# Kernel optimization log

Measured on AMD Instinct MI355X. Metric: run time of the kernel, lower is better.

The kernel has to match this reference:

```python
import jax, jax.numpy as jnp
import numpy as np

B, DIM, H, W = 8, 128, 64, 64
K = 7                      # involution kernel size
PAD = (K - 1) // 2
GC = 16                    # group_channels (RedNet involution default)
G = DIM // GC              # groups = 8
RED = 4                    # reduction_ratio
BN_EPS = 1e-5
LN_EPS = 1e-6


def setup_inputs() -> dict:
    key = jax.random.key(0)
    ks = jax.random.split(key, 8)
    s = lambda k, sh: jax.random.normal(k, sh, jnp.float32) * 0.02
    return {
        "x": jax.random.normal(ks[0], (B, DIM, H, W), jnp.float32),
        # involution kernel-generation branch: 1x1 conv -> BN -> ReLU -> 1x1 conv
        "conv1_w": s(ks[1], (DIM // RED, DIM)), "conv1_b": jnp.zeros((DIM // RED,), jnp.float32),
        "bn_g": jnp.ones((DIM // RED,), jnp.float32), "bn_b": jnp.zeros((DIM // RED,), jnp.float32),
        "bn_mean": jnp.zeros((DIM // RED,), jnp.float32), "bn_var": jnp.ones((DIM // RED,), jnp.float32),
        "conv2_w": s(ks[2], (K * K * G, DIM // RED)), "conv2_b": jnp.zeros((K * K * G,), jnp.float32),
        # LayerNorm (channels_last)
        "ln_g": jnp.ones((DIM,), jnp.float32), "ln_b": jnp.zeros((DIM,), jnp.float32),
        # pointwise MLP
        "pw1_w": s(ks[3], (2 * DIM, DIM)), "pw1_b": jnp.zeros((2 * DIM,), jnp.float32),
        "pw2_w": s(ks[4], (DIM, 2 * DIM)), "pw2_b": jnp.zeros((DIM,), jnp.float32),
    }


def _involution(x, conv1_w, conv1_b, bn_g, bn_b, bn_mean, bn_var, conv2_w, conv2_b):
    # kernel-generation: 1x1 conv -> BN(eval) -> ReLU -> 1x1 conv
    t = jnp.einsum('oc,bchw->bohw', conv1_w, x) + conv1_b[None, :, None, None]
    scale = bn_g * jax.lax.rsqrt(bn_var + BN_EPS)
    t = t * scale[None, :, None, None] + (bn_b - bn_mean * scale)[None, :, None, None]
    t = jax.nn.relu(t)
    wgt = jnp.einsum('oc,bchw->bohw', conv2_w, t) + conv2_b[None, :, None, None]
    wgt = wgt.reshape(B, G, K * K, H, W)            # per-pixel kernels
    # apply per-pixel kernel: accumulate over window offsets (no unfold materialization)
    xp = jnp.pad(x, ((0, 0), (0, 0), (PAD, PAD), (PAD, PAD)))
    xg = xp.reshape(B, G, GC, H + 2 * PAD, W + 2 * PAD)
    out = jnp.zeros((B, G, GC, H, W), x.dtype)
    for i in range(K):
        for j in range(K):
            patch = xg[:, :, :, i:i + H, j:j + W]   # [B,G,GC,H,W]
            out = out + wgt[:, :, i * K + j][:, :, None] * patch
    return out.reshape(B, DIM, H, W)


def reference(x, conv1_w, conv1_b, bn_g, bn_b, bn_mean, bn_var, conv2_w, conv2_b,
              ln_g, ln_b, pw1_w, pw1_b, pw2_w, pw2_b):
    identity = x
    y = _involution(x, conv1_w, conv1_b, bn_g, bn_b, bn_mean, bn_var, conv2_w, conv2_b)
    y = y.transpose(0, 2, 3, 1)                     # NCHW -> NHWC
    mu = jnp.mean(y, axis=-1, keepdims=True)
    var = jnp.var(y, axis=-1, keepdims=True)
    y = (y - mu) * jax.lax.rsqrt(var + LN_EPS) * ln_g + ln_b
    y = jnp.einsum('bhwc,fc->bhwf', y, pw1_w) + pw1_b
    y = jax.nn.gelu(y, approximate=False)           # torch nn.GELU default (erf)
    # dropout: inference mode -> identity
    y = jnp.einsum('bhwf,cf->bhwc', y, pw2_w) + pw2_b
    y = y.transpose(0, 3, 1, 2)                     # NHWC -> NCHW
    return y + identity
```

## Files before the change

### kernel.cpp

```cpp
#include <hip/hip_runtime.h>
#include <hip/hip_bf16.h>
#include <math.h>

#define Bn   8
#define DIM  128
#define Hs   64
#define Ws   64
#define PADn 3
#define GC   16
#define Gn   8
#define CMID 32
#define NW   392
#define NWP  416

typedef __bf16 bf16x8 __attribute__((ext_vector_type(8)));
typedef float  f32x4  __attribute__((ext_vector_type(4)));
typedef _Float16 h2v  __attribute__((ext_vector_type(2)));
typedef __fp16   fp16x2 __attribute__((ext_vector_type(2)));

__device__ __forceinline__ f32x4 mfma16(bf16x8 a, bf16x8 b, f32x4 c) {
    return __builtin_amdgcn_mfma_f32_16x16x32_bf16(a, b, c, 0, 0, 0);
}

__device__ __forceinline__ __bf16 tobf(float v) {
    __hip_bfloat16 h = __float2bfloat16(v);
    return *reinterpret_cast<__bf16*>(&h);
}

__device__ __forceinline__ unsigned su16(float f) {
    __hip_bfloat16 h = __float2bfloat16(f);
    return (unsigned)*reinterpret_cast<unsigned short*>(&h);
}

__device__ __forceinline__ unsigned pk2u(float a, float b) {
    fp16x2 p = __builtin_amdgcn_cvt_pkrtz(a, b);
    return __builtin_bit_cast(unsigned, p);
}

__device__ __forceinline__ float gelu_t(float v) {
    float u = 0.7978845608f * v * fmaf(0.044715f, v * v, 1.0f);
    float t = __builtin_amdgcn_exp2f(fminf(u, 30.f) * 2.885390082f);
    return v * t * __builtin_amdgcn_rcpf(t + 1.0f);
}

__global__ __launch_bounds__(256) void k0_cvt(const float* __restrict__ w1,
        const float* __restrict__ w2,
        const float* __restrict__ pw1, const float* __restrict__ pw2,
        const float* __restrict__ x,
        __hip_bfloat16* __restrict__ w1b, __hip_bfloat16* __restrict__ w2b,
        __hip_bfloat16* __restrict__ mw1b, __hip_bfloat16* __restrict__ mw2b,
        unsigned* __restrict__ xpair) {
    int T = blockIdx.x * 256 + threadIdx.x;
    if (T < 32768) {
        int i = T;
        if (i < CMID * DIM) w1b[i] = __float2bfloat16(w1[i]);
        if (i < NWP * CMID)
            w2b[i] = (i < NW * CMID) ? __float2bfloat16(w2[i]) : __float2bfloat16(0.f);
        {
            int f = i >> 7, j = i & 127;
            int qq = j >> 5, gg = (j >> 2) & 7, mm = j & 3;
            mw1b[i] = __float2bfloat16(pw1[f * 128 + gg * 16 + qq + 4 * mm]);
        }
        mw2b[i] = __float2bfloat16(pw2[i]);
    }
    int c8 = T >> 10;
    int p4 = (T & 1023) * 4;
    int bb = c8 >> 6, gg = (c8 >> 3) & 7, cc = c8 & 7;
    size_t src = ((size_t)(bb * DIM + gg * GC + cc)) * 4096 + p4;
    float4 lo = *(const float4*)&x[src];
    float4 hi = *(const float4*)&x[src + 8 * 4096];
    uint4 o;
    o.x = pk2u(lo.x, hi.x);
    o.y = pk2u(lo.y, hi.y);
    o.z = pk2u(lo.z, hi.z);
    o.w = pk2u(lo.w, hi.w);
    *(uint4*)&xpair[(size_t)c8 * 4096 + p4] = o;
}

__global__ __launch_bounds__(256) void k_all(const float* __restrict__ x,
        const unsigned* __restrict__ xpair,
        const __hip_bfloat16* __restrict__ w1b, const float* __restrict__ b1v,
        const float* __restrict__ bng, const float* __restrict__ bnb,
        const float* __restrict__ bnm, const float* __restrict__ bnv,
        const __hip_bfloat16* __restrict__ w2b, const float* __restrict__ b2v,
        const float* __restrict__ lng, const float* __restrict__ lnb,
        const __hip_bfloat16* __restrict__ mw1b, const float* __restrict__ mb1,
        const __hip_bfloat16* __restrict__ mw2b, const float* __restrict__ mb2,
        float* __restrict__ out) {
    __shared__ __align__(16) char uni[33792];
    __shared__ float ps[4][64], pss[4][64], mu_s[64], rs_s[64];
    h2v* xp    = (h2v*)uni;
    h2v* wgt2  = (h2v*)(uni + 16128);
    __hip_bfloat16* tsh = (__hip_bfloat16*)(uni + 29072);
    __hip_bfloat16* ylds = (__hip_bfloat16*)uni;
    __hip_bfloat16* zsh  = (__hip_bfloat16*)uni;

    int b = blockIdx.x & 7, h = blockIdx.x >> 3;
    int tid = threadIdx.x, lane = tid & 63, q = tid >> 6;
    int l15 = lane & 15, l4 = lane >> 4;
    int m0 = q * 16;

    int goff[16];
    unsigned ldsoPk[8];
#pragma unroll
    for (int e = 0; e < 16; ++e) {
        int i = tid + e * 256;
        int ccp = i / 490;
        int rem = i - ccp * 490;
        int r = rem / 70, col = rem - r * 70;
        int hh = h + r - PADn, wc = col - PADn;
        bool ok = (i < 3920) & ((unsigned)hh < (unsigned)Hs) & ((unsigned)wc < (unsigned)Ws);
        goff[e] = ok ? (ccp * 4096 + hh * 64 + wc) : -1;
        unsigned lo16 = (unsigned)(ccp * 504 + r * 72 + col);
        if ((e & 1) == 0) ldsoPk[e >> 1] = lo16;
        else              ldsoPk[e >> 1] |= lo16 << 16;
    }

    auto stage = [&](int g) {
        const unsigned* xg = xpair + (size_t)(b * 64 + g * 8) * 4096;
#pragma unroll
        for (int hf = 0; hf < 2; ++hf) {
            unsigned v[8];
#pragma unroll
            for (int e8 = 0; e8 < 8; ++e8) {
                int go = goff[hf * 8 + e8];
                v[e8] = (go >= 0) ? xg[go] : 0u;
            }
#pragma unroll
            for (int e8 = 0; e8 < 8; ++e8) {
                int e = hf * 8 + e8;
                if (e < 15 || tid < 80) {
                    unsigned ldso = (ldsoPk[e >> 1] >> ((e & 1) * 16)) & 0xFFFFu;
                    *(unsigned*)&xp[ldso] = v[e8];
                }
            }
        }
    };

    bf16x8 afr[4];
#pragma unroll
    for (int ks = 0; ks < 4; ++ks)
#pragma unroll
        for (int i = 0; i < 8; ++i) {
            int c = ks * 32 + l4 * 8 + i;
            afr[ks][i] = tobf(x[(((size_t)b * DIM + c) * Hs + h) * Ws + m0 + l15]);
        }
    f32x4 acc1[2];
    acc1[0] = (f32x4){0.f, 0.f, 0.f, 0.f};
    acc1[1] = (f32x4){0.f, 0.f, 0.f, 0.f};
#pragma unroll
    for (int nt = 0; nt < 2; ++nt)
#pragma unroll
        for (int ks = 0; ks < 4; ++ks) {
            bf16x8 bf = *(const bf16x8*)&w1b[(nt * 16 + l15) * DIM + ks * 32 + l4 * 8];
            acc1[nt] = mfma16(afr[ks], bf, acc1[nt]);
        }
#pragma unroll
    for (int nt = 0; nt < 2; ++nt) {
        int o = nt * 16 + l15;
        float sc = bng[o] * rsqrtf(bnv[o] + 1e-5f);
        float sh = bnb[o] - bnm[o] * sc;
        float bv = b1v[o];
#pragma unroll
        for (int r = 0; r < 4; ++r) {
            float v = (acc1[nt][r] + bv) * sc + sh;
            tsh[(m0 + l4 * 4 + r) * 34 + o] = __float2bfloat16(fmaxf(v, 0.f));
        }
    }
    __syncthreads();

    bf16x8 a_t = *(const bf16x8*)&tsh[(m0 + l15) * 34 + l4 * 8];

    unsigned ypk[16];
    float s = 0.f, ss = 0.f;

#pragma unroll 1
    for (int g = 0; g < Gn; ++g) {
        stage(g);
        {
            f32x4 ac[4];
#pragma unroll
            for (int nt = 0; nt < 4; ++nt) ac[nt] = (f32x4){0.f, 0.f, 0.f, 0.f};
#pragma unroll
            for (int nt = 0; nt < 4; ++nt) {
                bf16x8 bf = *(const bf16x8*)&w2b[(size_t)(g * 49 + nt * 16 + l15) * CMID + l4 * 8];
                ac[nt] = mfma16(a_t, bf, ac[nt]);
            }
#pragma unroll
            for (int nt = 0; nt < 4; ++nt) {
                int p = nt * 16 + l15;
                if (p < 49) {
                    float bias = b2v[g * 49 + p];
#pragma unroll
                    for (int r = 0; r < 4; ++r) {
                        _Float16 hf16 = (_Float16)(ac[nt][r] + bias);
                        wgt2[p * 66 + m0 + l4 * 4 + r] = (h2v){hf16, hf16};
                    }
                }
            }
        }
        __syncthreads();

        float a00 = 0.f, a01 = 0.f, a10 = 0.f, a11 = 0.f;
        {
            h2v wv[28];
#pragma unroll
            for (int p = 0; p < 28; ++p) wv[p] = wgt2[p * 66 + lane];
#pragma unroll
            for (int pi = 0; pi < 2; ++pi) {
                const h2v* xrow = xp + (q + pi * 4) * 504;
                float accx = 0.f, accy = 0.f;
#pragma unroll
                for (int r = 0; r < 4; ++r) {
                    h2v hacc = (h2v){(_Float16)0.f, (_Float16)0.f};
#pragma unroll
                    for (int j = 0; j < 7; ++j)
                        hacc = wv[r * 7 + j] * xrow[r * 72 + lane + j] + hacc;
                    accx += (float)hacc.x;
                    accy += (float)hacc.y;
                }
                if (pi == 0) { a00 = accx; a01 = accy; }
                else         { a10 = accx; a11 = accy; }
            }
        }
        {
            h2v wv[21];
#pragma unroll
            for (int p = 0; p < 21; ++p) wv[p] = wgt2[(28 + p) * 66 + lane];
#pragma unroll
            for (int pi = 0; pi < 2; ++pi) {
                const h2v* xrow = xp + (q + pi * 4) * 504;
                float accx = 0.f, accy = 0.f;
#pragma unroll
                for (int r = 0; r < 3; ++r) {
                    h2v hacc = (h2v){(_Float16)0.f, (_Float16)0.f};
#pragma unroll
                    for (int j = 0; j < 7; ++j)
                        hacc = wv[r * 7 + j] * xrow[(r + 4) * 72 + lane + j] + hacc;
                    accx += (float)hacc.x;
                    accy += (float)hacc.y;
                }
                if (pi == 0) { a00 += accx; a01 += accy; }
                else         { a10 += accx; a11 += accy; }
            }
        }
        ypk[g * 2]     = su16(a00) | (su16(a10) << 16);
        ypk[g * 2 + 1] = su16(a01) | (su16(a11) << 16);
        s += (a00 + a10) + (a01 + a11);
        ss = fmaf(a00, a00, fmaf(a10, a10, fmaf(a01, a01, fmaf(a11, a11, ss))));
        __syncthreads();
    }

    ps[q][lane] = s; pss[q][lane] = ss;
    __syncthreads();
    if (tid < 64) {
        float sa = ps[0][tid] + ps[1][tid] + ps[2][tid] + ps[3][tid];
        float sb = pss[0][tid] + pss[1][tid] + pss[2][tid] + pss[3][tid];
        float mu = sa * (1.f / DIM);
        float var = sb * (1.f / DIM) - mu * mu;
        mu_s[tid] = mu;
        rs_s[tid] = rsqrtf(var + 1e-6f);
    }
    __syncthreads();
    {
        float mu = mu_s[lane], rs = rs_s[lane];
        unsigned wds[16];
#pragma unroll
        for (int g = 0; g < 8; ++g)
#pragma unroll
            for (int hf = 0; hf < 2; ++hf) {
                unsigned wk = ypk[g * 2 + hf];
                float lo = __uint_as_float(wk << 16);
                float hi = __uint_as_float(wk & 0xffff0000u);
                int c0 = g * 16 + q + hf * 8, c1 = c0 + 4;
                lo = (lo - mu) * rs * lng[c0] + lnb[c0];
                hi = (hi - mu) * rs * lng[c1] + lnb[c1];
                wds[g * 2 + hf] = su16(lo) | (su16(hi) << 16);
            }
        __hip_bfloat16* dst = ylds + lane * 136 + q * 32;
#pragma unroll
        for (int c4 = 0; c4 < 4; ++c4) {
            uint4 vv;
            vv.x = wds[c4 * 4 + 0];
            vv.y = wds[c4 * 4 + 1];
            vv.z = wds[c4 * 4 + 2];
            vv.w = wds[c4 * 4 + 3];
            *(uint4*)&dst[c4 * 8] = vv;
        }
    }
    __syncthreads();

    bf16x8 ay[4];
#pragma unroll
    for (int ks = 0; ks < 4; ++ks)
        ay[ks] = *(const bf16x8*)&ylds[(m0 + l15) * 136 + ks * 32 + l4 * 8];
    __syncthreads();

    __hip_bfloat16* zw = zsh + q * 16 * 264;
#pragma unroll
    for (int half = 0; half < 2; ++half) {
        f32x4 zac[8];
#pragma unroll
        for (int n = 0; n < 8; ++n) zac[n] = (f32x4){0.f, 0.f, 0.f, 0.f};
#pragma unroll
        for (int ks = 0; ks < 4; ++ks)
#pragma unroll
            for (int n = 0; n < 8; ++n) {
                int nt = half * 8 + n;
                bf16x8 bf = *(const bf16x8*)&mw1b[(nt * 16 + l15) * DIM + ks * 32 + l4 * 8];
                zac[n] = mfma16(ay[ks], bf, zac[n]);
            }
#pragma unroll
        for (int n = 0; n < 8; ++n) {
            int nt = half * 8 + n;
            float bv = mb1[nt * 16 + l15];
#pragma unroll
            for (int r = 0; r < 4; ++r) {
                float v = gelu_t(zac[n][r] + bv);
                zw[(l4 * 4 + r) * 264 + nt * 16 + l15] = __float2bfloat16(v);
            }
        }
    }

    bf16x8 az[8];
#pragma unroll
    for (int ks = 0; ks < 8; ++ks)
        az[ks] = *(const bf16x8*)&zw[l15 * 264 + ks * 32 + l4 * 8];

    f32x4 oac[8];
#pragma unroll
    for (int n = 0; n < 8; ++n) oac[n] = (f32x4){0.f, 0.f, 0.f, 0.f};
#pragma unroll
    for (int ks = 0; ks < 8; ++ks)
#pragma unroll
        for (int n = 0; n < 8; ++n) {
            bf16x8 bf = *(const bf16x8*)&mw2b[(n * 16 + l15) * 256 + ks * 32 + l4 * 8];
            oac[n] = mfma16(az[ks], bf, oac[n]);
        }

    float4 xr[8];
#pragma unroll
    for (int n = 0; n < 8; ++n) {
        int c = n * 16 + l15;
        xr[n] = *(const float4*)&x[(((size_t)b * DIM + c) * Hs + h) * Ws + m0 + l4 * 4];
    }
#pragma unroll
    for (int n = 0; n < 8; ++n) {
        int c = n * 16 + l15;
        float bv = mb2[c];
        size_t gi = (((size_t)b * DIM + c) * Hs + h) * Ws + m0 + l4 * 4;
        float4 o;
        o.x = oac[n][0] + bv + xr[n].x;
        o.y = oac[n][1] + bv + xr[n].y;
        o.z = oac[n][2] + bv + xr[n].z;
        o.w = oac[n][3] + bv + xr[n].w;
        *(float4*)&out[gi] = o;
    }
}

extern "C" void kernel_launch(void* const* d_in, const int* in_sizes, int n_in,
                              void* d_out, int out_size, void* d_ws, size_t ws_size,
                              hipStream_t stream) {
    const float* x       = (const float*)d_in[0];
    const float* conv1_w = (const float*)d_in[1];
    const float* conv1_b = (const float*)d_in[2];
    const float* bn_g    = (const float*)d_in[3];
    const float* bn_b    = (const float*)d_in[4];
    const float* bn_mean = (const float*)d_in[5];
    const float* bn_var  = (const float*)d_in[6];
    const float* conv2_w = (const float*)d_in[7];
    const float* conv2_b = (const float*)d_in[8];
    const float* ln_g    = (const float*)d_in[9];
    const float* ln_b    = (const float*)d_in[10];
    const float* pw1_w   = (const float*)d_in[11];
    const float* pw1_b   = (const float*)d_in[12];
    const float* pw2_w   = (const float*)d_in[13];
    const float* pw2_b   = (const float*)d_in[14];
    float* out = (float*)d_out;

    char* ws = (char*)d_ws;
    __hip_bfloat16* w1b  = (__hip_bfloat16*)ws;
    __hip_bfloat16* w2b  = (__hip_bfloat16*)(ws + 8192);
    __hip_bfloat16* mw1b = (__hip_bfloat16*)(ws + 34816);
    __hip_bfloat16* mw2b = (__hip_bfloat16*)(ws + 100352);
    unsigned* xpair      = (unsigned*)(ws + (1 << 20));

    hipLaunchKernelGGL(k0_cvt, dim3(2048), dim3(256), 0, stream,
                       conv1_w, conv2_w, pw1_w, pw2_w, x,
                       w1b, w2b, mw1b, mw2b, xpair);
    hipLaunchKernelGGL(k_all, dim3(Bn * Hs), dim3(256), 0, stream,
                       x, xpair, w1b, conv1_b, bn_g, bn_b, bn_mean, bn_var,
                       w2b, conv2_b, ln_g, ln_b,
                       mw1b, pw1_b, mw2b, pw2_b, out);
}
```

Measured before the change: 72.14 us.

## Split fused kernel into single-wave blocks over 16-pixel row segments

The fused involution+LayerNorm+MLP kernel moves from one 256-thread block per image row to one 64-thread wavefront per 16-pixel segment of a row, giving four times as many blocks. All __syncthreads barriers and the cross-wave LayerNorm reduction are dropped in favour of wave shuffles. The x patch staging is double-buffered, with the first group staged before the first 1x1 conv. The LDS footprint shrinks, and the y tile uses an XOR swizzle with the MLP weight permutation changed to match. In exchange, each block now loads a haloed 22-wide window, so more x data is fetched redundantly. The kernel also relies on single-wave lockstep for LDS ordering and holds more registers per thread.

```diff
diff --git a/kernel.cpp b/kernel.cpp
--- a/kernel.cpp
+++ b/kernel.cpp
@@ -58,8 +58,9 @@
             w2b[i] = (i < NW * CMID) ? __float2bfloat16(w2[i]) : __float2bfloat16(0.f);
         {
             int f = i >> 7, j = i & 127;
-            int qq = j >> 5, gg = (j >> 2) & 7, mm = j & 3;
-            mw1b[i] = __float2bfloat16(pw1[f * 128 + gg * 16 + qq + 4 * mm]);
+            int t4 = j >> 5, k = j & 31;
+            int g = k >> 2, pi = (k >> 1) & 1, sel = k & 1;
+            mw1b[i] = __float2bfloat16(pw1[f * 128 + g * 16 + t4 * 2 + pi + 8 * sel]);
         }
         mw2b[i] = __float2bfloat16(pw2[i]);
     }
@@ -77,7 +78,7 @@
     *(uint4*)&xpair[(size_t)c8 * 4096 + p4] = o;
 }
 
-__global__ __launch_bounds__(256) void k_all(const float* __restrict__ x,
+__global__ __launch_bounds__(64) void k_all(const float* __restrict__ x,
         const unsigned* __restrict__ xpair,
         const __hip_bfloat16* __restrict__ w1b, const float* __restrict__ b1v,
         const float* __restrict__ bng, const float* __restrict__ bnb,
@@ -87,54 +88,46 @@
         const __hip_bfloat16* __restrict__ mw1b, const float* __restrict__ mb1,
         const __hip_bfloat16* __restrict__ mw2b, const float* __restrict__ mb2,
         float* __restrict__ out) {
-    __shared__ __align__(16) char uni[33792];
-    __shared__ float ps[4][64], pss[4][64], mu_s[64], rs_s[64];
+    __shared__ __align__(16) char uni[15368];
     h2v* xp    = (h2v*)uni;
-    h2v* wgt2  = (h2v*)(uni + 16128);
-    __hip_bfloat16* tsh = (__hip_bfloat16*)(uni + 29072);
+    h2v* wgt2  = (h2v*)(uni + 10752);
+    __hip_bfloat16* tsh = (__hip_bfloat16*)(uni + 14280);
     __hip_bfloat16* ylds = (__hip_bfloat16*)uni;
-    __hip_bfloat16* zsh  = (__hip_bfloat16*)uni;
-
-    int b = blockIdx.x & 7, h = blockIdx.x >> 3;
-    int tid = threadIdx.x, lane = tid & 63, q = tid >> 6;
+    __hip_bfloat16* zsh  = (__hip_bfloat16*)(uni + 4352);
+
+    int bid = blockIdx.x;
+    int b = bid & 7;
+    int rest = bid >> 3;
+    int h = rest >> 2, wq = rest & 3;
+    int w0 = wq * 16;
+    int lane = threadIdx.x;
     int l15 = lane & 15, l4 = lane >> 4;
-    int m0 = q * 16;
-
-    int goff[16];
-    unsigned ldsoPk[8];
-#pragma unroll
-    for (int e = 0; e < 16; ++e) {
-        int i = tid + e * 256;
-        int ccp = i / 490;
-        int rem = i - ccp * 490;
-        int r = rem / 70, col = rem - r * 70;
-        int hh = h + r - PADn, wc = col - PADn;
-        bool ok = (i < 3920) & ((unsigned)hh < (unsigned)Hs) & ((unsigned)wc < (unsigned)Ws);
+    int px = l15, t4 = l4;
+
+    int goff[20];
+    unsigned short ldso[20];
+#pragma unroll
+    for (int e = 0; e < 20; ++e) {
+        int i = lane + e * 64;
+        int ccp = i / 154;
+        int rem = i - ccp * 154;
+        int r = rem / 22, col = rem - r * 22;
+        int hh = h + r - PADn, wc = w0 + col - PADn;
+        bool ok = (i < 1232) & ((unsigned)hh < (unsigned)Hs) & ((unsigned)wc < (unsigned)Ws);
         goff[e] = ok ? (ccp * 4096 + hh * 64 + wc) : -1;
-        unsigned lo16 = (unsigned)(ccp * 504 + r * 72 + col);
-        if ((e & 1) == 0) ldsoPk[e >> 1] = lo16;
-        else              ldsoPk[e >> 1] |= lo16 << 16;
-    }
-
-    auto stage = [&](int g) {
+        ldso[e] = (unsigned short)(ccp * 168 + r * 24 + col);
+    }
+
+    auto stage = [&](int g, int buf) {
         const unsigned* xg = xpair + (size_t)(b * 64 + g * 8) * 4096;
-#pragma unroll
-        for (int hf = 0; hf < 2; ++hf) {
-            unsigned v[8];
-#pragma unroll
-            for (int e8 = 0; e8 < 8; ++e8) {
-                int go = goff[hf * 8 + e8];
-                v[e8] = (go >= 0) ? xg[go] : 0u;
-            }
-#pragma unroll
-            for (int e8 = 0; e8 < 8; ++e8) {
-                int e = hf * 8 + e8;
-                if (e < 15 || tid < 80) {
-                    unsigned ldso = (ldsoPk[e >> 1] >> ((e & 1) * 16)) & 0xFFFFu;
-                    *(unsigned*)&xp[ldso] = v[e8];
-                }
-            }
-        }
+        unsigned v[20];
+#pragma unroll
+        for (int e = 0; e < 20; ++e)
+            v[e] = (goff[e] >= 0) ? xg[goff[e]] : 0u;
+#pragma unroll
+        for (int e = 0; e < 20; ++e)
+            if (e < 19 || lane < 16)
+                *(unsigned*)&xp[buf * 1344 + ldso[e]] = v[e];
     };
 
     bf16x8 afr[4];
@@ -143,8 +136,11 @@
 #pragma unroll
         for (int i = 0; i < 8; ++i) {
             int c = ks * 32 + l4 * 8 + i;
-            afr[ks][i] = tobf(x[(((size_t)b * DIM + c) * Hs + h) * Ws + m0 + l15]);
-        }
+            afr[ks][i] = tobf(x[(((size_t)b * DIM + c) * Hs + h) * Ws + w0 + l15]);
+        }
+
+    stage(0, 0);
+
     f32x4 acc1[2];
     acc1[0] = (f32x4){0.f, 0.f, 0.f, 0.f};
     acc1[1] = (f32x4){0.f, 0.f, 0.f, 0.f};
@@ -164,19 +160,20 @@
 #pragma unroll
         for (int r = 0; r < 4; ++r) {
             float v = (acc1[nt][r] + bv) * sc + sh;
-            tsh[(m0 + l4 * 4 + r) * 34 + o] = __float2bfloat16(fmaxf(v, 0.f));
-        }
-    }
-    __syncthreads();
-
-    bf16x8 a_t = *(const bf16x8*)&tsh[(m0 + l15) * 34 + l4 * 8];
+            tsh[(l4 * 4 + r) * 34 + o] = __float2bfloat16(fmaxf(v, 0.f));
+        }
+    }
+    bf16x8 a_t = *(const bf16x8*)&tsh[l15 * 34 + l4 * 8];
 
     unsigned ypk[16];
     float s = 0.f, ss = 0.f;
 
 #pragma unroll 1
     for (int g = 0; g < Gn; ++g) {
-        stage(g);
+        int buf = g & 1;
+        if (g == 0) ;
+        else stage(g, buf);
+
         {
             f32x4 ac[4];
 #pragma unroll
@@ -194,90 +191,57 @@
 #pragma unroll
                     for (int r = 0; r < 4; ++r) {
                         _Float16 hf16 = (_Float16)(ac[nt][r] + bias);
-                        wgt2[p * 66 + m0 + l4 * 4 + r] = (h2v){hf16, hf16};
+                        wgt2[p * 18 + l4 * 4 + r] = (h2v){hf16, hf16};
                     }
                 }
             }
         }
-        __syncthreads();
-
-        float a00 = 0.f, a01 = 0.f, a10 = 0.f, a11 = 0.f;
-        {
-            h2v wv[28];
-#pragma unroll
-            for (int p = 0; p < 28; ++p) wv[p] = wgt2[p * 66 + lane];
+
+        h2v wv[49];
+#pragma unroll
+        for (int p = 0; p < 49; ++p) wv[p] = wgt2[p * 18 + px];
+
+#pragma unroll
+        for (int pi = 0; pi < 2; ++pi) {
+            int ccp = t4 * 2 + pi;
+            const h2v* xrow = xp + buf * 1344 + ccp * 168;
+            float accx = 0.f, accy = 0.f;
+#pragma unroll
+            for (int r = 0; r < 7; ++r) {
+                h2v hacc = (h2v){(_Float16)0.f, (_Float16)0.f};
+#pragma unroll
+                for (int j = 0; j < 7; ++j)
+                    hacc = wv[r * 7 + j] * xrow[r * 24 + px + j] + hacc;
+                accx += (float)hacc.x;
+                accy += (float)hacc.y;
+            }
+            ypk[g * 2 + pi] = su16(accx) | (su16(accy) << 16);
+            s += accx + accy;
+            ss = fmaf(accx, accx, fmaf(accy, accy, ss));
+        }
+    }
+
+    s += __shfl_xor(s, 16);  s += __shfl_xor(s, 32);
+    ss += __shfl_xor(ss, 16); ss += __shfl_xor(ss, 32);
+    float mu = s * (1.f / DIM);
+    float var = ss * (1.f / DIM) - mu * mu;
+    float rs = rsqrtf(var + 1e-6f);
+
+    {
+        unsigned wds[16];
+#pragma unroll
+        for (int g = 0; g < 8; ++g)
 #pragma unroll
             for (int pi = 0; pi < 2; ++pi) {
-                const h2v* xrow = xp + (q + pi * 4) * 504;
-                float accx = 0.f, accy = 0.f;
-#pragma unroll
-                for (int r = 0; r < 4; ++r) {
-                    h2v hacc = (h2v){(_Float16)0.f, (_Float16)0.f};
-#pragma unroll
-                    for (int j = 0; j < 7; ++j)
-                        hacc = wv[r * 7 + j] * xrow[r * 72 + lane + j] + hacc;
-                    accx += (float)hacc.x;
-                    accy += (float)hacc.y;
-                }
-                if (pi == 0) { a00 = accx; a01 = accy; }
-                else         { a10 = accx; a11 = accy; }
-            }
-        }
-        {
-            h2v wv[21];
-#pragma unroll
-            for (int p = 0; p < 21; ++p) wv[p] = wgt2[(28 + p) * 66 + lane];
-#pragma unroll
-            for (int pi = 0; pi < 2; ++pi) {
-                const h2v* xrow = xp + (q + pi * 4) * 504;
-                float accx = 0.f, accy = 0.f;
-#pragma unroll
-                for (int r = 0; r < 3; ++r) {
-                    h2v hacc = (h2v){(_Float16)0.f, (_Float16)0.f};
-#pragma unroll
-                    for (int j = 0; j < 7; ++j)
-                        hacc = wv[r * 7 + j] * xrow[(r + 4) * 72 + lane + j] + hacc;
-                    accx += (float)hacc.x;
-                    accy += (float)hacc.y;
-                }
-                if (pi == 0) { a00 += accx; a01 += accy; }
-                else         { a10 += accx; a11 += accy; }
-            }
-        }
-        ypk[g * 2]     = su16(a00) | (su16(a10) << 16);
-        ypk[g * 2 + 1] = su16(a01) | (su16(a11) << 16);
-        s += (a00 + a10) + (a01 + a11);
-        ss = fmaf(a00, a00, fmaf(a10, a10, fmaf(a01, a01, fmaf(a11, a11, ss))));
-        __syncthreads();
-    }
-
-    ps[q][lane] = s; pss[q][lane] = ss;
-    __syncthreads();
-    if (tid < 64) {
-        float sa = ps[0][tid] + ps[1][tid] + ps[2][tid] + ps[3][tid];
-        float sb = pss[0][tid] + pss[1][tid] + pss[2][tid] + pss[3][tid];
-        float mu = sa * (1.f / DIM);
-        float var = sb * (1.f / DIM) - mu * mu;
-        mu_s[tid] = mu;
-        rs_s[tid] = rsqrtf(var + 1e-6f);
-    }
-    __syncthreads();
-    {
-        float mu = mu_s[lane], rs = rs_s[lane];
-        unsigned wds[16];
-#pragma unroll
-        for (int g = 0; g < 8; ++g)
-#pragma unroll
-            for (int hf = 0; hf < 2; ++hf) {
-                unsigned wk = ypk[g * 2 + hf];
+                unsigned wk = ypk[g * 2 + pi];
                 float lo = __uint_as_float(wk << 16);
                 float hi = __uint_as_float(wk & 0xffff0000u);
-                int c0 = g * 16 + q + hf * 8, c1 = c0 + 4;
+                int c0 = g * 16 + t4 * 2 + pi, c1 = c0 + 8;
                 lo = (lo - mu) * rs * lng[c0] + lnb[c0];
                 hi = (hi - mu) * rs * lng[c1] + lnb[c1];
-                wds[g * 2 + hf] = su16(lo) | (su16(hi) << 16);
-            }
-        __hip_bfloat16* dst = ylds + lane * 136 + q * 32;
+                wds[g * 2 + pi] = su16(lo) | (su16(hi) << 16);
+            }
+        __hip_bfloat16* dst = ylds + px * 136 + t4 * 32;
 #pragma unroll
         for (int c4 = 0; c4 < 4; ++c4) {
             uint4 vv;
@@ -285,18 +249,15 @@
             vv.y = wds[c4 * 4 + 1];
             vv.z = wds[c4 * 4 + 2];
             vv.w = wds[c4 * 4 + 3];
-            *(uint4*)&dst[c4 * 8] = vv;
-        }
-    }
-    __syncthreads();
+            *(uint4*)&dst[(c4 ^ (px & 3)) << 3] = vv;
+        }
+    }
 
     bf16x8 ay[4];
 #pragma unroll
     for (int ks = 0; ks < 4; ++ks)
-        ay[ks] = *(const bf16x8*)&ylds[(m0 + l15) * 136 + ks * 32 + l4 * 8];
-    __syncthreads();
-
-    __hip_bfloat16* zw = zsh + q * 16 * 264;
+        ay[ks] = *(const bf16x8*)&ylds[l15 * 136 + ks * 32 + ((l4 ^ (l15 & 3)) << 3)];
+
 #pragma unroll
     for (int half = 0; half < 2; ++half) {
         f32x4 zac[8];
@@ -317,7 +278,7 @@
 #pragma unroll
             for (int r = 0; r < 4; ++r) {
                 float v = gelu_t(zac[n][r] + bv);
-                zw[(l4 * 4 + r) * 264 + nt * 16 + l15] = __float2bfloat16(v);
+                zsh[(l4 * 4 + r) * 264 + nt * 16 + l15] = __float2bfloat16(v);
             }
         }
     }
@@ -325,7 +286,7 @@
     bf16x8 az[8];
 #pragma unroll
     for (int ks = 0; ks < 8; ++ks)
-        az[ks] = *(const bf16x8*)&zw[l15 * 264 + ks * 32 + l4 * 8];
+        az[ks] = *(const bf16x8*)&zsh[l15 * 264 + ks * 32 + l4 * 8];
 
     f32x4 oac[8];
 #pragma unroll
@@ -342,13 +303,13 @@
 #pragma unroll
     for (int n = 0; n < 8; ++n) {
         int c = n * 16 + l15;
-        xr[n] = *(const float4*)&x[(((size_t)b * DIM + c) * Hs + h) * Ws + m0 + l4 * 4];
+        xr[n] = *(const float4*)&x[(((size_t)b * DIM + c) * Hs + h) * Ws + w0 + l4 * 4];
     }
 #pragma unroll
     for (int n = 0; n < 8; ++n) {
         int c = n * 16 + l15;
         float bv = mb2[c];
-        size_t gi = (((size_t)b * DIM + c) * Hs + h) * Ws + m0 + l4 * 4;
+        size_t gi = (((size_t)b * DIM + c) * Hs + h) * Ws + w0 + l4 * 4;
         float4 o;
         o.x = oac[n][0] + bv + xr[n].x;
         o.y = oac[n][1] + bv + xr[n].y;
@@ -388,7 +349,7 @@
     hipLaunchKernelGGL(k0_cvt, dim3(2048), dim3(256), 0, stream,
                        conv1_w, conv2_w, pw1_w, pw2_w, x,
                        w1b, w2b, mw1b, mw2b, xpair);
-    hipLaunchKernelGGL(k_all, dim3(Bn * Hs), dim3(256), 0, stream,
+    hipLaunchKernelGGL(k_all, dim3(Bn * Hs * 4), dim3(64), 0, stream,
                        x, xpair, w1b, conv1_b, bn_g, bn_b, bn_mean, bn_var,
                        w2b, conv2_b, ln_g, ln_b,
                        mw1b, pw1_b, mw2b, pw2_b, out);
```

Measured after the change: 70.60 us. 1.02x faster.
